# Kernel optimization log

Measured on AMD Instinct MI355X. Metric: run time of the kernel, lower is better.

## Reference

```python
import jax, jax.numpy as jnp
import numpy as np

B, H, S, D, KG = 1, 8, 1024, 64, 10

def setup_inputs() -> dict:
    key = jax.random.key(0)
    ks = jax.random.split(key, 16)
    n = jax.random.normal
    u = jax.random.uniform
    return {
        'Q': n(ks[0], (B, H, S, D), dtype=jnp.float32),
        'K': n(ks[1], (B, H, S, D), dtype=jnp.float32),
        'V': n(ks[2], (B, H, S, D), dtype=jnp.float32),
        'distance_matrix': u(ks[3], (B, H, S, S), dtype=jnp.float32) * 10.0,
        'energy_matrix': u(ks[4], (B, H, S, S), dtype=jnp.float32) * 5.0,
        'mask': jnp.ones((B, H, S, S), dtype=jnp.int32),
        'mu_D': n(ks[5], (KG,), dtype=jnp.float32),
        'sigma_D': u(ks[6], (KG,), dtype=jnp.float32) + 0.5,  # keep sigma positive
        'b_D': n(ks[7], (KG,), dtype=jnp.float32) * 0.1,
        'mu_E': n(ks[8], (KG,), dtype=jnp.float32),
        'sigma_E': u(ks[9], (KG,), dtype=jnp.float32) + 0.5,
        'b_E': n(ks[10], (KG,), dtype=jnp.float32) * 0.1,
        'W1': n(ks[11], (KG, KG), dtype=jnp.float32) / np.sqrt(KG),
        'b1': jnp.zeros((KG,), dtype=jnp.float32),
        'W2': n(ks[12], (1, KG), dtype=jnp.float32) / np.sqrt(KG),
        'b2': jnp.zeros((1,), dtype=jnp.float32),
    }


def _rbf_mlp_bias(x, b, mu, sigma, W1, b1, W2, b2):
    # x: [B,H,S,S] -> Gaussian RBF features over K kernels, then small MLP -> [B,H,S,S]
    z = (x[..., None] + b - mu) / sigma                      # [B,H,S,S,K]
    inv_norm = 1.0 / (jnp.sqrt(2.0 * jnp.pi) * sigma)
    psi = jnp.exp(-0.5 * z * z) * inv_norm                   # [B,H,S,S,K]
    h = jax.nn.gelu(jnp.einsum('bhijk,lk->bhijl', psi, W1) + b1, approximate=False)
    return (jnp.einsum('bhijk,lk->bhijl', h, W2) + b2)[..., 0]


def reference(Q, K, V, distance_matrix, energy_matrix, mask,
              mu_D, sigma_D, b_D, mu_E, sigma_E, b_E, W1, b1, W2, b2):
    d_model = Q.shape[-1]
    scores = jnp.einsum('bhid,bhjd->bhij', Q, K) / np.sqrt(d_model * 2)
    scores = scores + _rbf_mlp_bias(distance_matrix, b_D, mu_D, sigma_D, W1, b1, W2, b2)
    scores = scores + _rbf_mlp_bias(energy_matrix, b_E, mu_E, sigma_E, W1, b1, W2, b2)
    scores = jnp.where(mask == 0, jnp.float32(-1e9), scores)
    attn = jax.nn.softmax(scores, axis=-1)
    return jnp.einsum('bhij,bhjd->bhid', attn, V)
```

## Files before the change

kernel.cpp:

```cpp
#include <hip/hip_runtime.h>
#include <math.h>

#define Hn 8
#define Sn 1024
#define Dn 64
#define KG 10
#define KS 2

#define TN 2048
#define RD 10.25f
#define RE 5.125f

typedef __attribute__((ext_vector_type(8))) short bf16x8;
typedef __attribute__((ext_vector_type(4))) float f32x4;
typedef unsigned short u16;
typedef unsigned int u32;

__device__ inline float bf2f(u16 u) {
    union { u32 i; float f; } v;
    v.i = ((u32)u) << 16;
    return v.f;
}

__device__ inline u16 f2bf(float f) {
    union { float f; u32 i; } v;
    v.f = f;
    u32 i = v.i;
    return (u16)((i + 0x7FFFu + ((i >> 16) & 1u)) >> 16);
}

__device__ float bias_eval(float x,
                           const float* __restrict__ mu, const float* __restrict__ sg,
                           const float* __restrict__ bb,
                           const float* __restrict__ W1, const float* __restrict__ b1,
                           const float* __restrict__ W2, const float* __restrict__ b2) {
    const float inv_s2pi = 0.39894228040143267794f;
    float psi[KG];
#pragma unroll
    for (int k = 0; k < KG; k++) {
        float s = sg[k];
        float z = (x + bb[k] - mu[k]) / s;
        psi[k] = __expf(-0.5f * z * z) * (inv_s2pi / s);
    }
    float out = b2[0];
#pragma unroll
    for (int l = 0; l < KG; l++) {
        float a = b1[l];
#pragma unroll
        for (int k = 0; k < KG; k++) a += psi[k] * W1[l * KG + k];
        float g = 0.5f * a * (1.0f + erff(a * 0.70710678118654752440f));
        out += g * W2[l];
    }
    return out;
}

__global__ __launch_bounds__(256) void build_tables_kernel(
    const float* __restrict__ muD, const float* __restrict__ sgD, const float* __restrict__ bD,
    const float* __restrict__ muE, const float* __restrict__ sgE, const float* __restrict__ bE,
    const float* __restrict__ W1, const float* __restrict__ b1,
    const float* __restrict__ W2, const float* __restrict__ b2,
    u32* __restrict__ tab)
{
    int id = blockIdx.x * 256 + threadIdx.x;
    int which = (id >= TN);
    int idx = id & (TN - 1);
    float h = (which ? RE : RD) / (float)TN;
    float x0 = idx * h;
    float v0, v1;
    if (which) {
        v0 = bias_eval(x0,     muE, sgE, bE, W1, b1, W2, b2);
        v1 = bias_eval(x0 + h, muE, sgE, bE, W1, b1, W2, b2);
    } else {
        v0 = bias_eval(x0,     muD, sgD, bD, W1, b1, W2, b2);
        v1 = bias_eval(x0 + h, muD, sgD, bD, W1, b1, W2, b2);
    }
    tab[id] = (u32)f2bf(v0) | ((u32)f2bf(v1 - v0) << 16);
}

__global__ __launch_bounds__(256) void prep_kernel(
    const float* __restrict__ Q, const float* __restrict__ K, const float* __restrict__ V,
    u16* __restrict__ Qb, u16* __restrict__ Kb, u16* __restrict__ VTi)
{
    __shared__ float tile[64][68];
    const int wg = blockIdx.x, tid = threadIdx.x;

    if (wg < 1024) {
        int i = wg * 256 + tid;
        int arr = i >> 17;
        i &= (1 << 17) - 1;
        float4 v = ((const float4*)(arr ? K : Q))[i];
        ushort4 o;
        o.x = f2bf(v.x); o.y = f2bf(v.y); o.z = f2bf(v.z); o.w = f2bf(v.w);
        ((ushort4*)(arr ? Kb : Qb))[i] = o;
    } else {
        const int b  = wg - 1024;
        const int h  = b >> 4;
        const int s0 = (b & 15) * 64;
        const int rr = tid >> 4, cc = (tid & 15) * 4;
        const float* Vh = V + ((size_t)h * Sn + s0) * Dn;
#pragma unroll
        for (int i = 0; i < 4; i++) {
            float4 v = *(const float4*)(Vh + (size_t)(i * 16 + rr) * Dn + cc);
            tile[i * 16 + rr][cc]     = v.x;
            tile[i * 16 + rr][cc + 1] = v.y;
            tile[i * 16 + rr][cc + 2] = v.z;
            tile[i * 16 + rr][cc + 3] = v.w;
        }
        __syncthreads();
        u16* dst = VTi + (size_t)h * Dn * Sn + s0;
#pragma unroll
        for (int i = 0; i < 4; i++) {
            const int d = i * 16 + rr;
            u16 tmp[4];
#pragma unroll
            for (int j2 = 0; j2 < 4; j2++) {
                int sp = cc + j2;
                int q = (sp >> 3) & 3, j = sp & 7;
                int s = (sp & ~31) + q * 4 + (j & 3) + ((j >> 2) << 4);
                tmp[j2] = f2bf(tile[s][d]);
            }
            ushort4 o = {tmp[0], tmp[1], tmp[2], tmp[3]};
            *(ushort4*)(dst + (size_t)d * Sn + cc) = o;
        }
    }
}

__global__ __launch_bounds__(256, 4) void attn_part_kernel(
    const u16* __restrict__ Qb, const u16* __restrict__ Kb, const u16* __restrict__ VTi,
    const float* __restrict__ Dm, const float* __restrict__ Em, const int* __restrict__ Mk,
    const u32* __restrict__ gtab,
    float* __restrict__ Opart, float* __restrict__ Lpart)
{
    __shared__ union {
        u32 tab[2 * TN];
        struct { float O[4][16][68]; float L[4][16]; } f;
    } sU;

    const int tid = threadIdx.x;
    {
        const uint4* g4 = (const uint4*)gtab;
        uint4* s4 = (uint4*)sU.tab;
#pragma unroll
        for (int i = 0; i < 4; i++) s4[tid + 256 * i] = g4[tid + 256 * i];
    }
    __syncthreads();

    const int qb   = blockIdx.x;
    const int h    = blockIdx.y;
    const int ks   = blockIdx.z;
    const int q0   = qb * 16;
    const int wave = tid >> 6;
    const int lane = tid & 63;
    const int quad = lane >> 4;
    const int l16  = lane & 15;

    const u16* Qh = Qb  + (size_t)h * Sn * Dn;
    const u16* Kh = Kb  + (size_t)h * Sn * Dn;
    const u16* Vh = VTi + (size_t)h * Dn * Sn;
    const size_t rowoff = ((size_t)h * Sn + q0 + l16) * Sn;
    const float* Dr = Dm + rowoff;
    const float* Er = Em + rowoff;
    const int*   Mr = Mk + rowoff;

    const float invhD = (float)TN / RD;
    const float invhE = (float)TN / RE;
    const float scale = 0.08838834764831845f;

    const bf16x8 bQ0 = *(const bf16x8*)(Qh + (q0 + l16) * Dn + quad * 8);
    const bf16x8 bQ1 = *(const bf16x8*)(Qh + (q0 + l16) * Dn + 32 + quad * 8);

    f32x4 O0 = {0.f, 0.f, 0.f, 0.f}, O1 = O0, O2 = O0, O3 = O0;
    float l_r = 0.f;

    const int kbase = ks * (Sn / KS) + wave * 128;
    const u16* krb = Kh + (size_t)l16 * Dn + quad * 8;
    const u16* vrb = Vh + quad * 8;

    float4 pD0[2], pD1[2], pE0[2], pE1[2];
    {
        const int c = kbase + quad * 4;
        pD0[0] = *(const float4*)(Dr + c);
        pD1[0] = *(const float4*)(Dr + c + 16);
        pE0[0] = *(const float4*)(Er + c);
        pE1[0] = *(const float4*)(Er + c + 16);
    }

#pragma unroll
    for (int t = 0; t < 4; t++) {
        const int cur = t & 1, nxt = cur ^ 1;
        const int k0 = kbase + t * 32;

        if (t < 3) {
            const int c = k0 + 32 + quad * 4;
            pD0[nxt] = *(const float4*)(Dr + c);
            pD1[nxt] = *(const float4*)(Dr + c + 16);
            pE0[nxt] = *(const float4*)(Er + c);
            pE1[nxt] = *(const float4*)(Er + c + 16);
        }

        const int4 m0 = *(const int4*)(Mr + k0 + quad * 4);
        const int4 m1 = *(const int4*)(Mr + k0 + 16 + quad * 4);

        const u16* kr = krb + (size_t)k0 * Dn;
        const bf16x8 aK00 = *(const bf16x8*)(kr);
        const bf16x8 aK01 = *(const bf16x8*)(kr + 32);
        const bf16x8 aK10 = *(const bf16x8*)(kr + 16 * Dn);
        const bf16x8 aK11 = *(const bf16x8*)(kr + 16 * Dn + 32);

        const u16* vr = vrb + k0;
        const bf16x8 bV0 = *(const bf16x8*)(vr + (size_t)(l16)      * Sn);
        const bf16x8 bV1 = *(const bf16x8*)(vr + (size_t)(16 + l16) * Sn);
        const bf16x8 bV2 = *(const bf16x8*)(vr + (size_t)(32 + l16) * Sn);
        const bf16x8 bV3 = *(const bf16x8*)(vr + (size_t)(48 + l16) * Sn);

        f32x4 s0 = {0.f, 0.f, 0.f, 0.f}, s1 = s0;
        s0 = __builtin_amdgcn_mfma_f32_16x16x32_bf16(aK00, bQ0, s0, 0, 0, 0);
        s0 = __builtin_amdgcn_mfma_f32_16x16x32_bf16(aK01, bQ1, s0, 0, 0, 0);
        s1 = __builtin_amdgcn_mfma_f32_16x16x32_bf16(aK10, bQ0, s1, 0, 0, 0);
        s1 = __builtin_amdgcn_mfma_f32_16x16x32_bf16(aK11, bQ1, s1, 0, 0, 0);

        const float dv0[4] = {pD0[cur].x, pD0[cur].y, pD0[cur].z, pD0[cur].w};
        const float dv1[4] = {pD1[cur].x, pD1[cur].y, pD1[cur].z, pD1[cur].w};
        const float ev0[4] = {pE0[cur].x, pE0[cur].y, pE0[cur].z, pE0[cur].w};
        const float ev1[4] = {pE1[cur].x, pE1[cur].y, pE1[cur].z, pE1[cur].w};
        const int   mv0[4] = {m0.x, m0.y, m0.z, m0.w};
        const int   mv1[4] = {m1.x, m1.y, m1.z, m1.w};

        bf16x8 aP;
#pragma unroll
        for (int r = 0; r < 4; r++) {
            float tf = dv0[r] * invhD;
            int ix = min((int)tf, TN - 1);
            u32 p = sU.tab[ix];
            float b = fmaf(bf2f((u16)(p >> 16)), tf - (float)ix, bf2f((u16)p));
            tf = ev0[r] * invhE;
            ix = min((int)tf, TN - 1);
            p = sU.tab[TN + ix];
            b += fmaf(bf2f((u16)(p >> 16)), tf - (float)ix, bf2f((u16)p));
            b = fminf(fmaxf(b, -60.f), 64.f);
            float v0 = fmaf(s0[r], scale, b);
            v0 = (mv0[r] == 0) ? -60.f : v0;

            tf = dv1[r] * invhD;
            ix = min((int)tf, TN - 1);
            p = sU.tab[ix];
            b = fmaf(bf2f((u16)(p >> 16)), tf - (float)ix, bf2f((u16)p));
            tf = ev1[r] * invhE;
            ix = min((int)tf, TN - 1);
            p = sU.tab[TN + ix];
            b += fmaf(bf2f((u16)(p >> 16)), tf - (float)ix, bf2f((u16)p));
            b = fminf(fmaxf(b, -60.f), 64.f);
            float v1 = fmaf(s1[r], scale, b);
            v1 = (mv1[r] == 0) ? -60.f : v1;

            const float e0 = __expf(v0);
            const float e1 = __expf(v1);
            l_r += e0 + e1;
            aP[r]     = (short)f2bf(e0);
            aP[4 + r] = (short)f2bf(e1);
        }

        O0 = __builtin_amdgcn_mfma_f32_16x16x32_bf16(aP, bV0, O0, 0, 0, 0);
        O1 = __builtin_amdgcn_mfma_f32_16x16x32_bf16(aP, bV1, O1, 0, 0, 0);
        O2 = __builtin_amdgcn_mfma_f32_16x16x32_bf16(aP, bV2, O2, 0, 0, 0);
        O3 = __builtin_amdgcn_mfma_f32_16x16x32_bf16(aP, bV3, O3, 0, 0, 0);
    }

    l_r += __shfl_xor(l_r, 16, 64);
    l_r += __shfl_xor(l_r, 32, 64);
    __syncthreads();
    if (lane < 16) sU.f.L[wave][lane] = l_r;
#pragma unroll
    for (int r = 0; r < 4; r++) {
        sU.f.O[wave][quad * 4 + r][ 0 + l16] = O0[r];
        sU.f.O[wave][quad * 4 + r][16 + l16] = O1[r];
        sU.f.O[wave][quad * 4 + r][32 + l16] = O2[r];
        sU.f.O[wave][quad * 4 + r][48 + l16] = O3[r];
    }
    __syncthreads();

    const int row = tid >> 4;
    const int c4  = (tid & 15) * 4;
    const size_t pidx = ((size_t)ks * Hn + h) * (Sn / 16) + qb;

    float acc[4];
#pragma unroll
    for (int c = 0; c < 4; c++) {
        acc[c] = 0.f;
#pragma unroll
        for (int w = 0; w < 4; w++) acc[c] += sU.f.O[w][row][c4 + c];
    }
    float4 ov = {acc[0], acc[1], acc[2], acc[3]};
    *(float4*)(Opart + (pidx * 16 + row) * Dn + c4) = ov;

    if ((tid & 15) == 0) {
        float lg = 0.f;
#pragma unroll
        for (int w = 0; w < 4; w++) lg += sU.f.L[w][row];
        Lpart[pidx * 16 + row] = lg;
    }
}

__global__ __launch_bounds__(256) void combine_kernel(
    const float* __restrict__ Opart, const float* __restrict__ Lpart,
    float* __restrict__ out)
{
    const int qb  = blockIdx.x;
    const int h   = blockIdx.y;
    const int tid = threadIdx.x;
    const int row = tid >> 4;
    const int c4  = (tid & 15) * 4;

    float acc[4] = {0.f, 0.f, 0.f, 0.f};
    float lg = 0.f;
#pragma unroll
    for (int ks = 0; ks < KS; ks++) {
        const size_t pidx = ((size_t)ks * Hn + h) * (Sn / 16) + qb;
        const float4 o = *(const float4*)(Opart + (pidx * 16 + row) * Dn + c4);
        acc[0] += o.x; acc[1] += o.y; acc[2] += o.z; acc[3] += o.w;
        lg += Lpart[pidx * 16 + row];
    }
    const float inv = 1.0f / lg;
    float4 ov = {acc[0] * inv, acc[1] * inv, acc[2] * inv, acc[3] * inv};
    *(float4*)(out + ((size_t)(h * Sn + qb * 16 + row)) * Dn + c4) = ov;
}

extern "C" void kernel_launch(void* const* d_in, const int* in_sizes, int n_in,
                              void* d_out, int out_size, void* d_ws, size_t ws_size,
                              hipStream_t stream) {
    const float* Q    = (const float*)d_in[0];
    const float* K    = (const float*)d_in[1];
    const float* V    = (const float*)d_in[2];
    const float* Dm   = (const float*)d_in[3];
    const float* Em   = (const float*)d_in[4];
    const int*   Mask = (const int*)d_in[5];
    const float* muD  = (const float*)d_in[6];
    const float* sgD  = (const float*)d_in[7];
    const float* bD   = (const float*)d_in[8];
    const float* muE  = (const float*)d_in[9];
    const float* sgE  = (const float*)d_in[10];
    const float* bE   = (const float*)d_in[11];
    const float* W1   = (const float*)d_in[12];
    const float* b1   = (const float*)d_in[13];
    const float* W2   = (const float*)d_in[14];
    const float* b2   = (const float*)d_in[15];

    u32* tab = (u32*)d_ws;
    u16* Qb  = (u16*)((char*)d_ws + 2 * TN * 4);
    u16* Kb  = Qb + (size_t)Hn * Sn * Dn;
    u16* VTi = Kb + (size_t)Hn * Sn * Dn;
    float* Opart = (float*)(VTi + (size_t)Hn * Sn * Dn);
    float* Lpart = Opart + (size_t)KS * Hn * (Sn / 16) * 16 * Dn;

    build_tables_kernel<<<2 * TN / 256, 256, 0, stream>>>(
        muD, sgD, bD, muE, sgE, bE, W1, b1, W2, b2, tab);

    prep_kernel<<<1152, 256, 0, stream>>>(Q, K, V, Qb, Kb, VTi);

    dim3 grid(Sn / 16, Hn, KS);
    attn_part_kernel<<<grid, 256, 0, stream>>>(Qb, Kb, VTi, Dm, Em, Mask, tab,
                                               Opart, Lpart);

    dim3 cgrid(Sn / 16, Hn);
    combine_kernel<<<cgrid, 256, 0, stream>>>(Opart, Lpart, (float*)d_out);
}
```

Baseline: 181.3 us.

## Stage distance/energy/mask tiles via async LDS loads and drop key split

Removes the two-way key split and the combine kernel. Each block now covers all 1024 keys in 8 tiles, and the distance, energy and mask tiles are double-buffered into shared memory through global_load_lds async copies, with coalesced row-pair loads replacing per-lane strided float4 reads. The bias lookup table is also halved to 1024 entries per matrix, which coarsens the interpolation and may cost accuracy. In exchange the kernel runs half as many blocks, the occupancy hint drops to 2, and a block-wide barrier is added every tile.

```diff
diff --git a/kernel.cpp b/kernel.cpp
--- a/kernel.cpp
+++ b/kernel.cpp
@@ -5,11 +5,14 @@
 #define Sn 1024
 #define Dn 64
 #define KG 10
-#define KS 2
-
-#define TN 2048
+
+#define TN 1024
 #define RD 10.25f
 #define RE 5.125f
+
+#define PAIRB 1040
+#define SLABB (8 * PAIRB)
+#define BUFB  (3 * SLABB)
 
 typedef __attribute__((ext_vector_type(8))) short bf16x8;
 typedef __attribute__((ext_vector_type(4))) float f32x4;
@@ -27,6 +30,12 @@
     v.f = f;
     u32 i = v.i;
     return (u16)((i + 0x7FFFu + ((i >> 16) & 1u)) >> 16);
+}
+
+__device__ inline void async16(const void* g, void* lds) {
+    __builtin_amdgcn_global_load_lds(
+        (const __attribute__((address_space(1))) void*)g,
+        (__attribute__((address_space(3))) void*)lds, 16, 0, 0);
 }
 
 __device__ float bias_eval(float x,
@@ -125,43 +134,55 @@
     }
 }
 
-__global__ __launch_bounds__(256, 4) void attn_part_kernel(
+__global__ __launch_bounds__(256, 2) void attn_kernel(
     const u16* __restrict__ Qb, const u16* __restrict__ Kb, const u16* __restrict__ VTi,
     const float* __restrict__ Dm, const float* __restrict__ Em, const int* __restrict__ Mk,
-    const u32* __restrict__ gtab,
-    float* __restrict__ Opart, float* __restrict__ Lpart)
+    const u32* __restrict__ gtab, float* __restrict__ out)
 {
-    __shared__ union {
-        u32 tab[2 * TN];
+    __shared__ __align__(16) union {
+        char buf[2][BUFB];
         struct { float O[4][16][68]; float L[4][16]; } f;
-    } sU;
-
-    const int tid = threadIdx.x;
-    {
-        const uint4* g4 = (const uint4*)gtab;
-        uint4* s4 = (uint4*)sU.tab;
-#pragma unroll
-        for (int i = 0; i < 4; i++) s4[tid + 256 * i] = g4[tid + 256 * i];
-    }
-    __syncthreads();
-
-    const int qb   = blockIdx.x;
+    } sB;
+    __shared__ __align__(16) u32 sTab[2 * TN];
+
+    const int tid  = threadIdx.x;
     const int h    = blockIdx.y;
-    const int ks   = blockIdx.z;
-    const int q0   = qb * 16;
+    const int q0   = blockIdx.x * 16;
     const int wave = tid >> 6;
     const int lane = tid & 63;
     const int quad = lane >> 4;
     const int l16  = lane & 15;
 
+    {
+        const uint4* g4 = (const uint4*)gtab;
+        uint4* s4 = (uint4*)sTab;
+        s4[tid] = g4[tid];
+        s4[tid + 256] = g4[tid + 256];
+    }
+
+    const size_t rb = ((size_t)h * Sn + q0) * Sn;
+    const float* Dg = Dm + rb;
+    const float* Eg = Em + rb;
+    const int*   Mg = Mk + rb;
+
+    const int drow = lane >> 5;
+    const int dcol = (lane & 31) * 4;
+
+    auto stage = [&](int t, int b) {
+        char* bb = sB.buf[b];
+#pragma unroll
+        for (int pp = 0; pp < 2; pp++) {
+            const int p = wave * 2 + pp;
+            const size_t go = (size_t)(2 * p + drow) * Sn + (size_t)t * 128 + dcol;
+            async16(Dg + go, bb + (size_t)p * PAIRB);
+            async16(Eg + go, bb + SLABB + (size_t)p * PAIRB);
+            async16(Mg + go, bb + 2 * SLABB + (size_t)p * PAIRB);
+        }
+    };
+
     const u16* Qh = Qb  + (size_t)h * Sn * Dn;
     const u16* Kh = Kb  + (size_t)h * Sn * Dn;
     const u16* Vh = VTi + (size_t)h * Dn * Sn;
-    const size_t rowoff = ((size_t)h * Sn + q0 + l16) * Sn;
-    const float* Dr = Dm + rowoff;
-    const float* Er = Em + rowoff;
-    const int*   Mr = Mk + rowoff;
-
     const float invhD = (float)TN / RD;
     const float invhE = (float)TN / RE;
     const float scale = 0.08838834764831845f;
@@ -172,70 +193,63 @@
     f32x4 O0 = {0.f, 0.f, 0.f, 0.f}, O1 = O0, O2 = O0, O3 = O0;
     float l_r = 0.f;
 
-    const int kbase = ks * (Sn / KS) + wave * 128;
     const u16* krb = Kh + (size_t)l16 * Dn + quad * 8;
     const u16* vrb = Vh + quad * 8;
 
-    float4 pD0[2], pD1[2], pE0[2], pE1[2];
-    {
-        const int c = kbase + quad * 4;
-        pD0[0] = *(const float4*)(Dr + c);
-        pD1[0] = *(const float4*)(Dr + c + 16);
-        pE0[0] = *(const float4*)(Er + c);
-        pE1[0] = *(const float4*)(Er + c + 16);
-    }
-
-#pragma unroll
-    for (int t = 0; t < 4; t++) {
-        const int cur = t & 1, nxt = cur ^ 1;
-        const int k0 = kbase + t * 32;
-
-        if (t < 3) {
-            const int c = k0 + 32 + quad * 4;
-            pD0[nxt] = *(const float4*)(Dr + c);
-            pD1[nxt] = *(const float4*)(Dr + c + 16);
-            pE0[nxt] = *(const float4*)(Er + c);
-            pE1[nxt] = *(const float4*)(Er + c + 16);
-        }
-
-        const int4 m0 = *(const int4*)(Mr + k0 + quad * 4);
-        const int4 m1 = *(const int4*)(Mr + k0 + 16 + quad * 4);
+    const int co = (wave * 32 + quad * 4) * 4;
+    const int ro = (l16 >> 1) * PAIRB + (l16 & 1) * 512;
+
+    stage(0, 0);
+    __syncthreads();
+
+#pragma unroll
+    for (int t = 0; t < 8; t++) {
+        if (t < 7) stage(t + 1, (t + 1) & 1);
+
+        const int k0 = t * 128 + wave * 32;
 
         const u16* kr = krb + (size_t)k0 * Dn;
         const bf16x8 aK00 = *(const bf16x8*)(kr);
         const bf16x8 aK01 = *(const bf16x8*)(kr + 32);
         const bf16x8 aK10 = *(const bf16x8*)(kr + 16 * Dn);
         const bf16x8 aK11 = *(const bf16x8*)(kr + 16 * Dn + 32);
-
         const u16* vr = vrb + k0;
         const bf16x8 bV0 = *(const bf16x8*)(vr + (size_t)(l16)      * Sn);
         const bf16x8 bV1 = *(const bf16x8*)(vr + (size_t)(16 + l16) * Sn);
         const bf16x8 bV2 = *(const bf16x8*)(vr + (size_t)(32 + l16) * Sn);
         const bf16x8 bV3 = *(const bf16x8*)(vr + (size_t)(48 + l16) * Sn);
 
+        const char* bb = sB.buf[t & 1];
+        const float4 Dv0 = *(const float4*)(bb + ro + co);
+        const float4 Dv1 = *(const float4*)(bb + ro + co + 64);
+        const float4 Ev0 = *(const float4*)(bb + SLABB + ro + co);
+        const float4 Ev1 = *(const float4*)(bb + SLABB + ro + co + 64);
+        const int4   Mv0 = *(const int4*)(bb + 2 * SLABB + ro + co);
+        const int4   Mv1 = *(const int4*)(bb + 2 * SLABB + ro + co + 64);
+
         f32x4 s0 = {0.f, 0.f, 0.f, 0.f}, s1 = s0;
         s0 = __builtin_amdgcn_mfma_f32_16x16x32_bf16(aK00, bQ0, s0, 0, 0, 0);
         s0 = __builtin_amdgcn_mfma_f32_16x16x32_bf16(aK01, bQ1, s0, 0, 0, 0);
         s1 = __builtin_amdgcn_mfma_f32_16x16x32_bf16(aK10, bQ0, s1, 0, 0, 0);
         s1 = __builtin_amdgcn_mfma_f32_16x16x32_bf16(aK11, bQ1, s1, 0, 0, 0);
 
-        const float dv0[4] = {pD0[cur].x, pD0[cur].y, pD0[cur].z, pD0[cur].w};
-        const float dv1[4] = {pD1[cur].x, pD1[cur].y, pD1[cur].z, pD1[cur].w};
-        const float ev0[4] = {pE0[cur].x, pE0[cur].y, pE0[cur].z, pE0[cur].w};
-        const float ev1[4] = {pE1[cur].x, pE1[cur].y, pE1[cur].z, pE1[cur].w};
-        const int   mv0[4] = {m0.x, m0.y, m0.z, m0.w};
-        const int   mv1[4] = {m1.x, m1.y, m1.z, m1.w};
+        const float dv0[4] = {Dv0.x, Dv0.y, Dv0.z, Dv0.w};
+        const float dv1[4] = {Dv1.x, Dv1.y, Dv1.z, Dv1.w};
+        const float ev0[4] = {Ev0.x, Ev0.y, Ev0.z, Ev0.w};
+        const float ev1[4] = {Ev1.x, Ev1.y, Ev1.z, Ev1.w};
+        const int   mv0[4] = {Mv0.x, Mv0.y, Mv0.z, Mv0.w};
+        const int   mv1[4] = {Mv1.x, Mv1.y, Mv1.z, Mv1.w};
 
         bf16x8 aP;
 #pragma unroll
         for (int r = 0; r < 4; r++) {
             float tf = dv0[r] * invhD;
             int ix = min((int)tf, TN - 1);
-            u32 p = sU.tab[ix];
+            u32 p = sTab[ix];
             float b = fmaf(bf2f((u16)(p >> 16)), tf - (float)ix, bf2f((u16)p));
             tf = ev0[r] * invhE;
             ix = min((int)tf, TN - 1);
-            p = sU.tab[TN + ix];
+            p = sTab[TN + ix];
             b += fmaf(bf2f((u16)(p >> 16)), tf - (float)ix, bf2f((u16)p));
             b = fminf(fmaxf(b, -60.f), 64.f);
             float v0 = fmaf(s0[r], scale, b);
@@ -243,11 +257,11 @@
 
             tf = dv1[r] * invhD;
             ix = min((int)tf, TN - 1);
-            p = sU.tab[ix];
+            p = sTab[ix];
             b = fmaf(bf2f((u16)(p >> 16)), tf - (float)ix, bf2f((u16)p));
             tf = ev1[r] * invhE;
             ix = min((int)tf, TN - 1);
-            p = sU.tab[TN + ix];
+            p = sTab[TN + ix];
             b += fmaf(bf2f((u16)(p >> 16)), tf - (float)ix, bf2f((u16)p));
             b = fminf(fmaxf(b, -60.f), 64.f);
             float v1 = fmaf(s1[r], scale, b);
@@ -264,65 +278,39 @@
         O1 = __builtin_amdgcn_mfma_f32_16x16x32_bf16(aP, bV1, O1, 0, 0, 0);
         O2 = __builtin_amdgcn_mfma_f32_16x16x32_bf16(aP, bV2, O2, 0, 0, 0);
         O3 = __builtin_amdgcn_mfma_f32_16x16x32_bf16(aP, bV3, O3, 0, 0, 0);
+
+        __syncthreads();
     }
 
     l_r += __shfl_xor(l_r, 16, 64);
     l_r += __shfl_xor(l_r, 32, 64);
-    __syncthreads();
-    if (lane < 16) sU.f.L[wave][lane] = l_r;
+    if (lane < 16) sB.f.L[wave][lane] = l_r;
 #pragma unroll
     for (int r = 0; r < 4; r++) {
-        sU.f.O[wave][quad * 4 + r][ 0 + l16] = O0[r];
-        sU.f.O[wave][quad * 4 + r][16 + l16] = O1[r];
-        sU.f.O[wave][quad * 4 + r][32 + l16] = O2[r];
-        sU.f.O[wave][quad * 4 + r][48 + l16] = O3[r];
+        sB.f.O[wave][quad * 4 + r][ 0 + l16] = O0[r];
+        sB.f.O[wave][quad * 4 + r][16 + l16] = O1[r];
+        sB.f.O[wave][quad * 4 + r][32 + l16] = O2[r];
+        sB.f.O[wave][quad * 4 + r][48 + l16] = O3[r];
     }
     __syncthreads();
 
     const int row = tid >> 4;
     const int c4  = (tid & 15) * 4;
-    const size_t pidx = ((size_t)ks * Hn + h) * (Sn / 16) + qb;
+    float lg = 0.f;
+#pragma unroll
+    for (int w = 0; w < 4; w++) lg += sB.f.L[w][row];
+    const float inv = 1.0f / lg;
 
     float acc[4];
 #pragma unroll
     for (int c = 0; c < 4; c++) {
         acc[c] = 0.f;
 #pragma unroll
-        for (int w = 0; w < 4; w++) acc[c] += sU.f.O[w][row][c4 + c];
+        for (int w = 0; w < 4; w++) acc[c] += sB.f.O[w][row][c4 + c];
+        acc[c] *= inv;
     }
     float4 ov = {acc[0], acc[1], acc[2], acc[3]};
-    *(float4*)(Opart + (pidx * 16 + row) * Dn + c4) = ov;
-
-    if ((tid & 15) == 0) {
-        float lg = 0.f;
-#pragma unroll
-        for (int w = 0; w < 4; w++) lg += sU.f.L[w][row];
-        Lpart[pidx * 16 + row] = lg;
-    }
-}
-
-__global__ __launch_bounds__(256) void combine_kernel(
-    const float* __restrict__ Opart, const float* __restrict__ Lpart,
-    float* __restrict__ out)
-{
-    const int qb  = blockIdx.x;
-    const int h   = blockIdx.y;
-    const int tid = threadIdx.x;
-    const int row = tid >> 4;
-    const int c4  = (tid & 15) * 4;
-
-    float acc[4] = {0.f, 0.f, 0.f, 0.f};
-    float lg = 0.f;
-#pragma unroll
-    for (int ks = 0; ks < KS; ks++) {
-        const size_t pidx = ((size_t)ks * Hn + h) * (Sn / 16) + qb;
-        const float4 o = *(const float4*)(Opart + (pidx * 16 + row) * Dn + c4);
-        acc[0] += o.x; acc[1] += o.y; acc[2] += o.z; acc[3] += o.w;
-        lg += Lpart[pidx * 16 + row];
-    }
-    const float inv = 1.0f / lg;
-    float4 ov = {acc[0] * inv, acc[1] * inv, acc[2] * inv, acc[3] * inv};
-    *(float4*)(out + ((size_t)(h * Sn + qb * 16 + row)) * Dn + c4) = ov;
+    *(float4*)(out + ((size_t)(h * Sn + q0 + row)) * Dn + c4) = ov;
 }
 
 extern "C" void kernel_launch(void* const* d_in, const int* in_sizes, int n_in,
@@ -349,18 +337,13 @@
     u16* Qb  = (u16*)((char*)d_ws + 2 * TN * 4);
     u16* Kb  = Qb + (size_t)Hn * Sn * Dn;
     u16* VTi = Kb + (size_t)Hn * Sn * Dn;
-    float* Opart = (float*)(VTi + (size_t)Hn * Sn * Dn);
-    float* Lpart = Opart + (size_t)KS * Hn * (Sn / 16) * 16 * Dn;
 
     build_tables_kernel<<<2 * TN / 256, 256, 0, stream>>>(
         muD, sgD, bD, muE, sgE, bE, W1, b1, W2, b2, tab);
 
     prep_kernel<<<1152, 256, 0, stream>>>(Q, K, V, Qb, Kb, VTi);
 
-    dim3 grid(Sn / 16, Hn, KS);
-    attn_part_kernel<<<grid, 256, 0, stream>>>(Qb, Kb, VTi, Dm, Em, Mask, tab,
-                                               Opart, Lpart);
-
-    dim3 cgrid(Sn / 16, Hn);
-    combine_kernel<<<cgrid, 256, 0, stream>>>(Opart, Lpart, (float*)d_out);
-}
+    dim3 grid(Sn / 16, Hn);
+    attn_kernel<<<grid, 256, 0, stream>>>(Qb, Kb, VTi, Dm, Em, Mask, tab,
+                                          (float*)d_out);
+}
```

New measurement: 173.1 us. -4.5%, faster.
